# Performance work log

Measured on AMD Instinct MI355X. Metric: run time of the kernel, lower is better.

Reference implementation:

```python
import jax, jax.numpy as jnp
import numpy as np

NC = 80            # number of classes (COCO)
NM = 32            # mask coefficients (YOLOv5-seg)
D = 4 + 1 + NC + NM
N_ANCHORS = 100800  # 1280x1280 input, strides 8/16/32, 3 anchors
CONF_THRES = 0.25
IOU_THRES = 0.45
MAX_DET = 300
TOPK = 4096        # fixed pre-NMS candidate budget (jit-compatible stand-in for boolean filter)


def setup_inputs() -> dict:
    key = jax.random.key(0)
    x = jax.random.uniform(key, (1, N_ANCHORS, D), dtype=jnp.float32)
    return {"x": x}


def _pairwise_iou(boxes):
    # boxes: [K, 4] in (y1, x1, y2, x2)
    y1, x1, y2, x2 = boxes[:, 0], boxes[:, 1], boxes[:, 2], boxes[:, 3]
    area = (y2 - y1) * (x2 - x1)
    iy1 = jnp.maximum(y1[:, None], y1[None, :])
    ix1 = jnp.maximum(x1[:, None], x1[None, :])
    iy2 = jnp.minimum(y2[:, None], y2[None, :])
    ix2 = jnp.minimum(x2[:, None], x2[None, :])
    inter = jnp.clip(iy2 - iy1, 0.0) * jnp.clip(ix2 - ix1, 0.0)
    union = area[:, None] + area[None, :] - inter
    return inter / jnp.maximum(union, 1e-9)


def reference(x):
    p = x[0]                                   # [N, D] (loop returns after first image)
    obj = p[:, 4]
    valid = obj > CONF_THRES                   # candidates = obj score > conf_thres
    cls_scores = p[:, 5:5 + NC] * obj[:, None] # scores = cls * obj
    scores = jnp.max(cls_scores, axis=1)
    classes = jnp.argmax(cls_scores, axis=1).astype(x.dtype)
    # xywh (center) -> yxyx
    xc, yc, w, h = p[:, 0], p[:, 1], p[:, 2], p[:, 3]
    yxyx = jnp.stack([yc - h * 0.5, xc - w * 0.5, yc + h * 0.5, xc + w * 0.5], axis=1)
    masks = p[:, 5 + NC:]                      # [N, NM]
    # replace torch's boolean-filter gather with fixed-size top-K over masked scores
    scores_m = jnp.where(valid, scores, -1.0)
    top_s, top_i = jax.lax.top_k(scores_m, TOPK)   # sorted desc, as torchvision nms requires
    b = yxyx[top_i]                            # [K, 4]
    keep0 = top_s > -0.5                       # only real candidates
    iou = _pairwise_iou(b)                     # [K, K]
    j_idx = jnp.arange(TOPK)

    def body(i, keep):
        sup = keep[i] & (iou[i] > IOU_THRES) & (j_idx > i)
        return keep & ~sup

    keep = jax.lax.fori_loop(0, TOPK, body, keep0)
    # pad/select top MAX_DET surviving detections (score -1.0 marks padding)
    sel_s = jnp.where(keep, top_s, -1.0)
    out_s, out_i = jax.lax.top_k(sel_s, MAX_DET)
    gi = top_i[out_i]
    return (yxyx[gi][None], classes[gi][None], out_s[None], masks[gi][None])
```

## Files before the change

kernel.cpp:

```cpp
#include <hip/hip_runtime.h>


constexpr int    N_ANCH = 100800;
constexpr int    DIMV   = 117;
constexpr int    NCLS   = 80;
constexpr int    TOPKN  = 4096;
constexpr int    MAXDET = 300;
constexpr int    KCAP   = 12288;
constexpr int    NBUCK  = 16384;
constexpr int    NSLICE = 32;

constexpr size_t WS_HIST   = 0;
constexpr size_t WS_SCORES = WS_HIST   + 65536ull * 4;
constexpr size_t WS_CLS    = WS_SCORES + 100800ull * 4;
constexpr size_t WS_SEL    = WS_CLS    + 100800ull * 4;
constexpr size_t WS_KEYS   = WS_SEL    + 256;
constexpr size_t WS_RANK   = WS_KEYS   + (size_t)KCAP * 8;
constexpr size_t WS_SIDX   = WS_RANK   + (size_t)KCAP * 4;
constexpr size_t WS_SSC    = WS_SIDX   + 4096ull * 4;
constexpr size_t WS_BOXES  = WS_SSC    + 4096ull * 4;
constexpr size_t WS_MASK   = WS_BOXES  + 4096ull * 16;
constexpr size_t WS_OUTI   = WS_MASK   + 4096ull * 64 * 8;
constexpr size_t WS_OUTS   = WS_OUTI   + 1200;

__global__ void zero_kernel(unsigned* __restrict__ slices, int* __restrict__ sel,
                            int* __restrict__ rank) {
    int i = blockIdx.x * blockDim.x + threadIdx.x;
    if (i < NSLICE * NBUCK) slices[i] = 0u;
    if (i < KCAP)           rank[i]  = 0;
    if (i < 64)             sel[i]   = 0;
}

constexpr int SROWS = 64;
__global__ void score_kernel(const float* __restrict__ x, float* __restrict__ scores,
                             int* __restrict__ cls, unsigned* __restrict__ slices) {
    __shared__ float sx[SROWS * DIMV];
    int block0 = blockIdx.x * SROWS;
    const float4* src = (const float4*)(x + (size_t)block0 * DIMV);
    float4* dst = (float4*)sx;
    constexpr int NV4 = SROWS * DIMV / 4;
    for (int i = threadIdx.x; i < NV4; i += 128) dst[i] = src[i];
    __syncthreads();
    int row  = threadIdx.x >> 1;
    int half = threadIdx.x & 1;
    const float* rp = sx + row * DIMV;
    float obj = rp[4];
    const float* cp = rp + 5 + half * 40;
    float best = -1.0f;
    int   bc   = half * 40;
#pragma unroll 8
    for (int c = 0; c < 40; ++c) {
        float s = __fmul_rn(cp[c], obj);
        if (s > best) { best = s; bc = half * 40 + c; }
    }
    float so = __shfl_xor(best, 1);
    int   co = __shfl_xor(bc, 1);
    if (half == 0) {
        if (so > best) { best = so; bc = co; }
        int a = block0 + row;
        bool valid = obj > 0.25f;
        scores[a] = valid ? best : -1.0f;
        cls[a]    = bc;
        if (valid) {
            unsigned b = __float_as_uint(best) >> 16;
            atomicAdd(&slices[(blockIdx.x & (NSLICE - 1)) * NBUCK + b], 1u);
        }
    }
}

__global__ void reduce_hist_kernel(const unsigned* __restrict__ slices,
                                   unsigned* __restrict__ hist) {
    int b = blockIdx.x * 256 + threadIdx.x;
    unsigned s = 0;
#pragma unroll
    for (int k = 0; k < NSLICE; ++k) s += slices[k * NBUCK + b];
    hist[b] = s;
}

__global__ void select_kernel(const unsigned* __restrict__ hist, int* sel) {
    __shared__ unsigned sv[1024];
    int t = threadIdx.x;
    int base = NBUCK - 16 * (t + 1);
    const uint4* hp = (const uint4*)(hist + base);
    unsigned own = 0;
#pragma unroll
    for (int k = 0; k < 4; ++k) {
        uint4 v = hp[k];
        own += v.x + v.y + v.z + v.w;
    }
    sv[t] = own;
    __syncthreads();
    for (int off = 1; off < 1024; off <<= 1) {
        unsigned v = (t >= off) ? sv[t - off] : 0u;
        __syncthreads();
        sv[t] += v;
        __syncthreads();
    }
    unsigned incl = sv[t];
    unsigned before = incl - own;
    if (before < (unsigned)TOPKN && incl >= (unsigned)TOPKN) {
        unsigned running = before;
        for (int k = 15; k >= 0; --k) {
            unsigned h = hist[base + k];
            running += h;
            if (running >= (unsigned)TOPKN) {
                sel[0] = base + k;
                sel[1] = (int)(running - h);
                break;
            }
        }
    }
}

__global__ void compact_kernel(const float* __restrict__ scores, int* sel,
                               unsigned long long* __restrict__ keys) {
    int a = blockIdx.x * blockDim.x + threadIdx.x;
    if (a >= N_ANCH) return;
    float s = scores[a];
    if (s < 0.0f) return;
    unsigned bits = __float_as_uint(s);
    if ((int)(bits >> 16) < sel[0]) return;
    int pos = atomicAdd(&sel[2], 1);
    if (pos < KCAP) keys[pos] = ((unsigned long long)bits << 32) | (unsigned)(~a);
}

constexpr int NCOLP = 4;
__global__ void rank_kernel(const unsigned long long* __restrict__ keys,
                            const int* __restrict__ sel, int* __restrict__ rank) {
    __shared__ unsigned long long tile[2048];
    int n = sel[2]; if (n > KCAP) n = KCAP;
    int i = blockIdx.x * 256 + threadIdx.x;
    unsigned long long myKey = (i < n) ? keys[i] : 0ull;
    int cnt = 0;
    for (int t0 = blockIdx.y * 2048; t0 < n; t0 += 2048 * NCOLP) {
        int m = n - t0; if (m > 2048) m = 2048;
        for (int j = threadIdx.x; j < m; j += 256) tile[j] = keys[t0 + j];
        __syncthreads();
        int j = 0;
        for (; j + 3 < m; j += 4) {
            cnt += (tile[j]     > myKey);
            cnt += (tile[j + 1] > myKey);
            cnt += (tile[j + 2] > myKey);
            cnt += (tile[j + 3] > myKey);
        }
        for (; j < m; ++j) cnt += (tile[j] > myKey);
        __syncthreads();
    }
    if (i < n && cnt < TOPKN) atomicAdd(&rank[i], cnt);
}

__global__ void scatter_kernel(const float* __restrict__ x,
                               const unsigned long long* __restrict__ keys,
                               const int* __restrict__ sel, const int* __restrict__ rank,
                               int* __restrict__ sidx, float* __restrict__ sscore,
                               float* __restrict__ boxes) {
    int n = sel[2]; if (n > KCAP) n = KCAP;
    int i = blockIdx.x * 256 + threadIdx.x;
    if (i >= n) return;
    int r = rank[i];
    if (r >= TOPKN) return;
    unsigned long long k = keys[i];
    int a = (int)(~(unsigned)(k & 0xFFFFFFFFull));
    sidx[r]   = a;
    sscore[r] = __uint_as_float((unsigned)(k >> 32));
    const float* p = x + (size_t)a * DIMV;
    float xc = p[0], yc = p[1], w = p[2], h = p[3];
    float hw = __fmul_rn(w, 0.5f);
    float hh = __fmul_rn(h, 0.5f);
    boxes[r * 4 + 0] = __fsub_rn(yc, hh);
    boxes[r * 4 + 1] = __fsub_rn(xc, hw);
    boxes[r * 4 + 2] = __fadd_rn(yc, hh);
    boxes[r * 4 + 3] = __fadd_rn(xc, hw);
}

__global__ void iou_mask_kernel(const float* __restrict__ boxes,
                                unsigned long long* __restrict__ mask) {
    int colT = blockIdx.x, rowT = blockIdx.y;
    int t = threadIdx.x;
    int r = rowT * 64 + t;
    if (colT < rowT) {
        mask[(size_t)r * 64 + colT] = 0ull;
        return;
    }
    __shared__ float cb[64][5];
    int cj = colT * 64 + t;
    {
        float y1 = boxes[cj * 4 + 0], x1 = boxes[cj * 4 + 1];
        float y2 = boxes[cj * 4 + 2], x2 = boxes[cj * 4 + 3];
        cb[t][0] = y1; cb[t][1] = x1; cb[t][2] = y2; cb[t][3] = x2;
        cb[t][4] = __fmul_rn(__fsub_rn(y2, y1), __fsub_rn(x2, x1));
    }
    __syncthreads();
    float ry1 = boxes[r * 4 + 0], rx1 = boxes[r * 4 + 1];
    float ry2 = boxes[r * 4 + 2], rx2 = boxes[r * 4 + 3];
    float rarea = __fmul_rn(__fsub_rn(ry2, ry1), __fsub_rn(rx2, rx1));
    unsigned long long bitsw = 0ull;
#pragma unroll 8
    for (int j = 0; j < 64; ++j) {
        float iy1 = fmaxf(ry1, cb[j][0]);
        float ix1 = fmaxf(rx1, cb[j][1]);
        float iy2 = fminf(ry2, cb[j][2]);
        float ix2 = fminf(rx2, cb[j][3]);
        float ih = fmaxf(__fsub_rn(iy2, iy1), 0.0f);
        float iw = fmaxf(__fsub_rn(ix2, ix1), 0.0f);
        float inter = __fmul_rn(ih, iw);
        float uni = __fsub_rn(__fadd_rn(rarea, cb[j][4]), inter);
        float iou = __fdiv_rn(inter, fmaxf(uni, 1e-9f));
        if (iou > 0.45f && (colT * 64 + j) > r) bitsw |= (1ull << j);
    }
    mask[(size_t)r * 64 + colT] = bitsw;
}

#define NEXT_CAND(rX)                                              \
    {                                                              \
        while (candRem == 0ull && curWord < 63) {                  \
            ++curWord;                                             \
            candRem = __shfl(~remv, curWord);                      \
        }                                                          \
        if (candRem != 0ull) {                                     \
            int b_ = (int)__builtin_ctzll(candRem);                \
            candRem &= candRem - 1;                                \
            rX = (curWord << 6) + b_;                              \
        } else {                                                   \
            rX = -1;                                               \
        }                                                          \
    }

#define DECIDE(rX, mX)                                             \
    if ((rX) >= 0 && count < MAXDET) {                             \
        unsigned long long bal_ =                                  \
            __ballot(((remv >> ((rX) & 63)) & 1ull) != 0);         \
        if (!((bal_ >> ((rX) >> 6)) & 1ull)) {                     \
            if (lane == 0) keepArr[count] = (rX);                  \
            count++;                                               \
            remv |= (mX);                                          \
        }                                                          \
    }

__global__ void __launch_bounds__(64, 1)
nms_scan_kernel(const unsigned long long* __restrict__ mask,
                const float* __restrict__ sscore,
                int* __restrict__ outIdx, float* __restrict__ outScore) {
    int lane = threadIdx.x;
    unsigned long long remv = 0ull;
    __shared__ int keepArr[MAXDET];
    __shared__ unsigned long long remvFinal[64];
    int count = 0;

    int curWord = 0;
    unsigned long long candRem = ~0ull;

    int r0, r1, r2, r3;
    NEXT_CAND(r0); NEXT_CAND(r1); NEXT_CAND(r2); NEXT_CAND(r3);
    unsigned long long m0 = (r0 >= 0) ? mask[(size_t)r0 * 64 + lane] : 0ull;
    unsigned long long m1 = (r1 >= 0) ? mask[(size_t)r1 * 64 + lane] : 0ull;
    unsigned long long m2 = (r2 >= 0) ? mask[(size_t)r2 * 64 + lane] : 0ull;
    unsigned long long m3 = (r3 >= 0) ? mask[(size_t)r3 * 64 + lane] : 0ull;

    while (r0 >= 0 && count < MAXDET) {
        int s0, s1, s2, s3;
        NEXT_CAND(s0); NEXT_CAND(s1); NEXT_CAND(s2); NEXT_CAND(s3);
        unsigned long long n0 = (s0 >= 0) ? mask[(size_t)s0 * 64 + lane] : 0ull;
        unsigned long long n1 = (s1 >= 0) ? mask[(size_t)s1 * 64 + lane] : 0ull;
        unsigned long long n2 = (s2 >= 0) ? mask[(size_t)s2 * 64 + lane] : 0ull;
        unsigned long long n3 = (s3 >= 0) ? mask[(size_t)s3 * 64 + lane] : 0ull;
        DECIDE(r0, m0); DECIDE(r1, m1); DECIDE(r2, m2); DECIDE(r3, m3);
        r0 = s0; r1 = s1; r2 = s2; r3 = s3;
        m0 = n0; m1 = n1; m2 = n2; m3 = n3;
    }

    remvFinal[lane] = remv;
    __syncthreads();
    int K = count;
    for (int k = lane; k < K; k += 64) {
        int s = keepArr[k];
        outIdx[k] = s;
        outScore[k] = sscore[s];
    }
    if (K < MAXDET && lane == 0) {
        int filled = K;
        for (int w = 0; w < 64 && filled < MAXDET; ++w) {
            unsigned long long word = remvFinal[w];
            while (word && filled < MAXDET) {
                int b = (int)__builtin_ctzll(word);
                word &= word - 1;
                outIdx[filled] = (w << 6) + b;
                outScore[filled] = -1.0f;
                filled++;
            }
        }
    }
}

__global__ void write_out_kernel(const float* __restrict__ x, const int* __restrict__ sidx,
                                 const int* __restrict__ cls, const float* __restrict__ boxes,
                                 const int* __restrict__ outIdx, const float* __restrict__ outScore,
                                 float* __restrict__ out) {
    int o = blockIdx.x;
    int t = threadIdx.x;
    int s = outIdx[o];
    int a = sidx[s];
    if (t < 32) {
        out[1800 + o * 32 + t] = x[(size_t)a * DIMV + 85 + t];
    } else if (t < 36) {
        out[o * 4 + (t - 32)] = boxes[s * 4 + (t - 32)];
    } else if (t == 36) {
        out[1200 + o] = (float)cls[a];
    } else if (t == 37) {
        out[1500 + o] = outScore[o];
    }
}

extern "C" void kernel_launch(void* const* d_in, const int* in_sizes, int n_in,
                              void* d_out, int out_size, void* d_ws, size_t ws_size,
                              hipStream_t stream) {
    const float* x = (const float*)d_in[0];
    char* ws = (char*)d_ws;
    unsigned*            hist   = (unsigned*)(ws + WS_HIST);
    float*               scores = (float*)(ws + WS_SCORES);
    int*                 cls    = (int*)(ws + WS_CLS);
    int*                 sel    = (int*)(ws + WS_SEL);
    unsigned long long*  keys   = (unsigned long long*)(ws + WS_KEYS);
    int*                 rank   = (int*)(ws + WS_RANK);
    int*                 sidx   = (int*)(ws + WS_SIDX);
    float*               sscore = (float*)(ws + WS_SSC);
    float*               boxes  = (float*)(ws + WS_BOXES);
    unsigned long long*  mask   = (unsigned long long*)(ws + WS_MASK);
    unsigned*            slices = (unsigned*)(ws + WS_MASK);
    int*                 outIdx = (int*)(ws + WS_OUTI);
    float*               outSc  = (float*)(ws + WS_OUTS);

    zero_kernel<<<(NSLICE * NBUCK + 255) / 256, 256, 0, stream>>>(slices, sel, rank);
    score_kernel<<<N_ANCH / SROWS, 128, 0, stream>>>(x, scores, cls, slices);
    reduce_hist_kernel<<<NBUCK / 256, 256, 0, stream>>>(slices, hist);
    select_kernel<<<1, 1024, 0, stream>>>(hist, sel);
    compact_kernel<<<(N_ANCH + 255) / 256, 256, 0, stream>>>(scores, sel, keys);
    dim3 rg(KCAP / 256, NCOLP);
    rank_kernel<<<rg, 256, 0, stream>>>(keys, sel, rank);
    scatter_kernel<<<KCAP / 256, 256, 0, stream>>>(x, keys, sel, rank, sidx, sscore, boxes);
    dim3 mg(64, 64);
    iou_mask_kernel<<<mg, 64, 0, stream>>>(boxes, mask);
    nms_scan_kernel<<<1, 64, 0, stream>>>(mask, sscore, outIdx, outSc);
    write_out_kernel<<<MAXDET, 64, 0, stream>>>(x, sidx, cls, boxes, outIdx, outSc, (float*)d_out);
}
```

Before: 237.2 us.

## Restructure NMS scan into per-word blocks using LDS-cached diagonal masks

The IoU kernel now also writes each 64x64 diagonal block of the suppression mask to a separate buffer. The scan kernel loads those blocks into LDS and resolves keeps inside each 64-candidate word with register shuffles, with no ballot per candidate. It then ORs in the global mask rows of the kept candidates, four loads at a time. This takes global-memory latency off the serial decision chain, at the cost of an extra 32KB LDS preload and a per-word loop even for words with no live candidates.

```diff
diff --git a/kernel.cpp b/kernel.cpp
--- a/kernel.cpp
+++ b/kernel.cpp
@@ -22,6 +22,7 @@
 constexpr size_t WS_MASK   = WS_BOXES  + 4096ull * 16;
 constexpr size_t WS_OUTI   = WS_MASK   + 4096ull * 64 * 8;
 constexpr size_t WS_OUTS   = WS_OUTI   + 1200;
+constexpr size_t WS_DIAG   = WS_OUTS   + 1200;
 
 __global__ void zero_kernel(unsigned* __restrict__ slices, int* __restrict__ sel,
                             int* __restrict__ rank) {
@@ -174,7 +175,8 @@
 }
 
 __global__ void iou_mask_kernel(const float* __restrict__ boxes,
-                                unsigned long long* __restrict__ mask) {
+                                unsigned long long* __restrict__ mask,
+                                unsigned long long* __restrict__ diag) {
     int colT = blockIdx.x, rowT = blockIdx.y;
     int t = threadIdx.x;
     int r = rowT * 64 + t;
@@ -209,64 +211,52 @@
         if (iou > 0.45f && (colT * 64 + j) > r) bitsw |= (1ull << j);
     }
     mask[(size_t)r * 64 + colT] = bitsw;
-}
-
-#define NEXT_CAND(rX)                                              \
-    {                                                              \
-        while (candRem == 0ull && curWord < 63) {                  \
-            ++curWord;                                             \
-            candRem = __shfl(~remv, curWord);                      \
-        }                                                          \
-        if (candRem != 0ull) {                                     \
-            int b_ = (int)__builtin_ctzll(candRem);                \
-            candRem &= candRem - 1;                                \
-            rX = (curWord << 6) + b_;                              \
-        } else {                                                   \
-            rX = -1;                                               \
-        }                                                          \
-    }
-
-#define DECIDE(rX, mX)                                             \
-    if ((rX) >= 0 && count < MAXDET) {                             \
-        unsigned long long bal_ =                                  \
-            __ballot(((remv >> ((rX) & 63)) & 1ull) != 0);         \
-        if (!((bal_ >> ((rX) >> 6)) & 1ull)) {                     \
-            if (lane == 0) keepArr[count] = (rX);                  \
-            count++;                                               \
-            remv |= (mX);                                          \
-        }                                                          \
-    }
+    if (colT == rowT) diag[rowT * 64 + t] = bitsw;
+}
 
 __global__ void __launch_bounds__(64, 1)
 nms_scan_kernel(const unsigned long long* __restrict__ mask,
+                const unsigned long long* __restrict__ diag,
                 const float* __restrict__ sscore,
                 int* __restrict__ outIdx, float* __restrict__ outScore) {
     int lane = threadIdx.x;
-    unsigned long long remv = 0ull;
+    __shared__ unsigned long long diagLDS[64 * 64];
     __shared__ int keepArr[MAXDET];
     __shared__ unsigned long long remvFinal[64];
+    for (int i = lane; i < 64 * 64; i += 64) diagLDS[i] = diag[i];
+    unsigned long long remv = 0ull;
     int count = 0;
-
-    int curWord = 0;
-    unsigned long long candRem = ~0ull;
-
-    int r0, r1, r2, r3;
-    NEXT_CAND(r0); NEXT_CAND(r1); NEXT_CAND(r2); NEXT_CAND(r3);
-    unsigned long long m0 = (r0 >= 0) ? mask[(size_t)r0 * 64 + lane] : 0ull;
-    unsigned long long m1 = (r1 >= 0) ? mask[(size_t)r1 * 64 + lane] : 0ull;
-    unsigned long long m2 = (r2 >= 0) ? mask[(size_t)r2 * 64 + lane] : 0ull;
-    unsigned long long m3 = (r3 >= 0) ? mask[(size_t)r3 * 64 + lane] : 0ull;
-
-    while (r0 >= 0 && count < MAXDET) {
-        int s0, s1, s2, s3;
-        NEXT_CAND(s0); NEXT_CAND(s1); NEXT_CAND(s2); NEXT_CAND(s3);
-        unsigned long long n0 = (s0 >= 0) ? mask[(size_t)s0 * 64 + lane] : 0ull;
-        unsigned long long n1 = (s1 >= 0) ? mask[(size_t)s1 * 64 + lane] : 0ull;
-        unsigned long long n2 = (s2 >= 0) ? mask[(size_t)s2 * 64 + lane] : 0ull;
-        unsigned long long n3 = (s3 >= 0) ? mask[(size_t)s3 * 64 + lane] : 0ull;
-        DECIDE(r0, m0); DECIDE(r1, m1); DECIDE(r2, m2); DECIDE(r3, m3);
-        r0 = s0; r1 = s1; r2 = s2; r3 = s3;
-        m0 = n0; m1 = n1; m2 = n2; m3 = n3;
+    __syncthreads();
+
+    for (int w = 0; w < 64; ++w) {
+        unsigned long long ext = __shfl(remv, w);
+        unsigned long long alive = ~ext;
+        if (!alive) continue;
+        unsigned long long intraRow = diagLDS[w * 64 + lane];
+        unsigned long long kept = 0ull;
+        while (alive && count < MAXDET) {
+            int b = (int)__builtin_ctzll(alive);
+            kept |= (1ull << b);
+            if (lane == 0) keepArr[count] = (w << 6) + b;
+            count++;
+            unsigned long long suppB = __shfl(intraRow, b);
+            alive &= ~(suppB | (1ull << b));
+        }
+        if (count >= MAXDET) break;
+        unsigned long long km = kept;
+        const unsigned long long* base = mask + (((size_t)w << 6) << 6) + lane;
+        while (km) {
+            int b0 = (int)__builtin_ctzll(km); km &= km - 1;
+            int b1 = b0, b2 = b0, b3 = b0;
+            if (km) { b1 = (int)__builtin_ctzll(km); km &= km - 1; }
+            if (km) { b2 = (int)__builtin_ctzll(km); km &= km - 1; }
+            if (km) { b3 = (int)__builtin_ctzll(km); km &= km - 1; }
+            unsigned long long l0 = base[(size_t)b0 * 64];
+            unsigned long long l1 = base[(size_t)b1 * 64];
+            unsigned long long l2 = base[(size_t)b2 * 64];
+            unsigned long long l3 = base[(size_t)b3 * 64];
+            remv |= (l0 | l1) | (l2 | l3);
+        }
     }
 
     remvFinal[lane] = remv;
@@ -329,6 +319,7 @@
     unsigned*            slices = (unsigned*)(ws + WS_MASK);
     int*                 outIdx = (int*)(ws + WS_OUTI);
     float*               outSc  = (float*)(ws + WS_OUTS);
+    unsigned long long*  diag   = (unsigned long long*)(ws + WS_DIAG);
 
     zero_kernel<<<(NSLICE * NBUCK + 255) / 256, 256, 0, stream>>>(slices, sel, rank);
     score_kernel<<<N_ANCH / SROWS, 128, 0, stream>>>(x, scores, cls, slices);
@@ -339,7 +330,7 @@
     rank_kernel<<<rg, 256, 0, stream>>>(keys, sel, rank);
     scatter_kernel<<<KCAP / 256, 256, 0, stream>>>(x, keys, sel, rank, sidx, sscore, boxes);
     dim3 mg(64, 64);
-    iou_mask_kernel<<<mg, 64, 0, stream>>>(boxes, mask);
-    nms_scan_kernel<<<1, 64, 0, stream>>>(mask, sscore, outIdx, outSc);
+    iou_mask_kernel<<<mg, 64, 0, stream>>>(boxes, mask, diag);
+    nms_scan_kernel<<<1, 64, 0, stream>>>(mask, diag, sscore, outIdx, outSc);
     write_out_kernel<<<MAXDET, 64, 0, stream>>>(x, sidx, cls, boxes, outIdx, outSc, (float*)d_out);
 }
```

New measurement: 257.4 us. 8.5% more time.
